# Kernel optimization log

Measured on AMD Instinct MI355X. Metric: run time of the kernel, lower is better.

The kernel has to match this reference:

```python
import jax, jax.numpy as jnp
import numpy as np

OUT = 7            # output_size per dim
RATIO = 2          # sampling_ratio
CANON_S = 160.0    # canonical_scale
CANON_L = 4.0      # canonical_level
EPS = 1e-6
K_MIN, K_MAX = 2, 5                      # from scales 1/4 .. 1/32
SCALES = (0.25, 0.125, 0.0625, 0.03125)  # inferred vs 256^3 image


def _coords(start, bsz):
    # start,bsz: [N] -> sample coords [N, OUT*RATIO]
    offs = (jnp.arange(OUT)[:, None] + (jnp.arange(RATIO) + 0.5) / RATIO).reshape(-1)
    return start[:, None] + offs[None, :] * bsz[:, None]


def _axis(c, dim):
    # torchvision border handling: zero outside [-1, dim], clamp inside
    valid = ((c > -1.0) & (c < dim)).astype(c.dtype)
    cc = jnp.clip(c, 0.0, dim - 1.0)
    lo = jnp.floor(cc).astype(jnp.int32)
    hi = jnp.minimum(lo + 1, int(dim) - 1)
    frac = cc - lo
    return lo, hi, (1.0 - frac) * valid, frac * valid


def roi_align_3d(feat, batch_idx, boxes, scale):
    # feat [B,C,X,Y,Z]; boxes [N,6] = (x1,y1,z1,x2,y2,z2) in image coords
    N = boxes.shape[0]
    C = feat.shape[1]
    dims = feat.shape[2:]
    start = boxes[:, :3] * scale
    size = jnp.maximum(boxes[:, 3:] * scale - start, 1.0)
    bsz = size / OUT  # [N,3] bin sizes
    f = jnp.transpose(feat, (0, 2, 3, 4, 1))  # [B,X,Y,Z,C]
    ax = [_axis(_coords(start[:, d], bsz[:, d]), float(dims[d])) for d in range(3)]
    b = batch_idx
    acc = jnp.zeros((N, OUT * RATIO, OUT * RATIO, OUT * RATIO, C), feat.dtype)
    for ix, wx in ((ax[0][0], ax[0][2]), (ax[0][1], ax[0][3])):
        for iy, wy in ((ax[1][0], ax[1][2]), (ax[1][1], ax[1][3])):
            for iz, wz in ((ax[2][0], ax[2][2]), (ax[2][1], ax[2][3])):
                v = f[b[:, None, None, None], ix[:, :, None, None],
                      iy[:, None, :, None], iz[:, None, None, :]]  # [N,Sx,Sy,Sz,C]
                w = wx[:, :, None, None] * wy[:, None, :, None] * wz[:, None, None, :]
                acc = acc + w[..., None] * v
    # average sampling points within each bin
    acc = acc.reshape(N, OUT, RATIO, OUT, RATIO, OUT, RATIO, C).mean(axis=(2, 4, 6))
    return jnp.transpose(acc, (0, 4, 1, 2, 3))  # [N,C,OUT,OUT,OUT]


def level_map(boxes):
    vol = ((boxes[:, 3] - boxes[:, 0]) * (boxes[:, 4] - boxes[:, 1])
           * (boxes[:, 5] - boxes[:, 2]))
    s = jnp.cbrt(vol)
    lvl = jnp.floor(CANON_L + jnp.log2(s / CANON_S) + EPS)
    return jnp.clip(lvl, K_MIN, K_MAX).astype(jnp.int32) - K_MIN


def setup_inputs() -> dict:
    key = jax.random.key(0)
    ks = jax.random.split(key, 6)
    N, C = 256, 64
    feat0 = jax.random.normal(ks[0], (1, C, 64, 64, 64), jnp.float32)
    feat1 = jax.random.normal(ks[1], (1, C, 32, 32, 32), jnp.float32)
    feat2 = jax.random.normal(ks[2], (1, C, 16, 16, 16), jnp.float32)
    feat3 = jax.random.normal(ks[3], (1, C, 8, 8, 8), jnp.float32)
    sz = 10.0 + jax.random.uniform(ks[4], (N, 3)) * 240.0   # edge lengths
    p1 = jax.random.uniform(ks[5], (N, 3)) * (256.0 - sz)
    boxes = jnp.concatenate([p1, p1 + sz], axis=1)  # valid (x1<x2 etc.) in 256^3 image
    return {"feat0": feat0, "feat1": feat1, "feat2": feat2, "feat3": feat3, "boxes": boxes}


def reference(feat0, feat1, feat2, feat3, boxes):
    feats = (feat0, feat1, feat2, feat3)
    levels = level_map(boxes)
    b = jnp.zeros(boxes.shape[0], dtype=jnp.int32)  # single image -> all batch id 0
    out = jnp.zeros((boxes.shape[0], feat0.shape[1], OUT, OUT, OUT), feat0.dtype)
    for l, (feat, sc) in enumerate(zip(feats, SCALES)):
        pooled = roi_align_3d(feat, b, boxes, sc)
        mask = (levels == l).astype(pooled.dtype)[:, None, None, None, None]
        out = out + mask * pooled
    return out
```

## Files before the change

### kernel.cpp

```cpp
#include <hip/hip_runtime.h>
#include <math.h>

#define OUT 7
#define NVOX 343
#define VB 32
#define NCH2 11

typedef unsigned short u16;
typedef unsigned int u32;

__device__ __forceinline__ u16 f32_to_bf16(float f) {
    u32 u = __float_as_uint(f);
    u32 r = (u + 0x7fffu + ((u >> 16) & 1u)) >> 16;
    return (u16)r;
}
__device__ __forceinline__ float bf16_to_f32(u16 h) {
    return __uint_as_float(((u32)h) << 16);
}

__device__ __forceinline__ void axis_samp(float c, float fdim, int dim,
                                          int& lo, float& w0, float& w1) {
    float valid = (c > -1.0f && c < fdim) ? 1.0f : 0.0f;
    float cc = fminf(fmaxf(c, 0.0f), fdim - 1.0f);
    lo = (int)floorf(cc);
    float fr = cc - (float)lo;
    w0 = (1.0f - fr) * valid;
    w1 = fr * valid;
}

__device__ __forceinline__ void box_setup(const float* bp,
                                          int d0, int d1, int d2_, int d3,
                                          int& l, int& dim, float& fdim,
                                          float& st0, float& st1, float& st2,
                                          float& bs0, float& bs1, float& bs2) {
    float b0 = bp[0], b1 = bp[1], b2 = bp[2];
    float b3 = bp[3], b4 = bp[4], b5 = bp[5];
    float vol = (b3 - b0) * (b4 - b1) * (b5 - b2);
    float s = cbrtf(vol);
    float lvl = floorf(4.0f + log2f(s / 160.0f) + 1e-6f);
    lvl = fminf(fmaxf(lvl, 2.0f), 5.0f);
    l = (int)lvl - 2;
    float scale;
    if (l == 0)      { dim = d0;  scale = 0.25f;    }
    else if (l == 1) { dim = d1;  scale = 0.125f;   }
    else if (l == 2) { dim = d2_; scale = 0.0625f;  }
    else             { dim = d3;  scale = 0.03125f; }
    fdim = (float)dim;
    st0 = b0 * scale; st1 = b1 * scale; st2 = b2 * scale;
    float e0 = fmaxf(b3 * scale - st0, 1.0f);
    float e1 = fmaxf(b4 * scale - st1, 1.0f);
    float e2 = fmaxf(b5 * scale - st2, 1.0f);
    bs0 = e0 * (1.0f / OUT); bs1 = e1 * (1.0f / OUT); bs2 = e2 * (1.0f / OUT);
}

#define LDSF 11776
#define FBLK 512

__global__ __launch_bounds__(FBLK) void roi_align_fallback_kernel(
    const float* __restrict__ f0, const float* __restrict__ f1,
    const float* __restrict__ f2, const float* __restrict__ f3,
    const float* __restrict__ boxes, float* __restrict__ out,
    int N, int C, int d0, int d1, int d2_, int d3)
{
    __shared__ float lds[LDSF];
    const int c   = blockIdx.x;
    const int n   = blockIdx.y;
    const int tid = threadIdx.x;

    int l, dim; float fdim, st0, st1, st2, bs0, bs1, bs2;
    box_setup(boxes + n * 6, d0, d1, d2_, d3,
              l, dim, fdim, st0, st1, st2, bs0, bs1, bs2);
    const float* f = (l == 0) ? f0 : (l == 1) ? f1 : (l == 2) ? f2 : f3;

    const int dsq = dim * dim;
    const size_t dcube = (size_t)dim * dsq;
    const float* fc = f + (size_t)c * dcube;

    int x0 = (int)floorf(fminf(fmaxf(st0 + 0.25f * bs0, 0.0f), fdim - 1.0f));
    int x1 = min((int)floorf(fminf(fmaxf(st0 + 6.75f * bs0, 0.0f), fdim - 1.0f)) + 1, dim - 1);
    int y0 = (int)floorf(fminf(fmaxf(st1 + 0.25f * bs1, 0.0f), fdim - 1.0f));
    int y1 = min((int)floorf(fminf(fmaxf(st1 + 6.75f * bs1, 0.0f), fdim - 1.0f)) + 1, dim - 1);
    int z0 = (int)floorf(fminf(fmaxf(st2 + 0.25f * bs2, 0.0f), fdim - 1.0f));
    int z1 = min((int)floorf(fminf(fmaxf(st2 + 6.75f * bs2, 0.0f), fdim - 1.0f)) + 1, dim - 1);

    int nx = x1 - x0 + 1, ny = y1 - y0 + 1, nz = z1 - z0 + 1;
    int nzp = nz + 1;
    int nynzp = ny * nzp;
    int nrows = nx * ny;
    int nregp = nrows * nzp;

    int xl[2], yl[2], zl[2];
    float xw0[2], xw1[2], yw0[2], yw1[2], zw0[2], zw1[2];
    if (tid < NVOX) {
        int oz = tid % OUT;
        int oy = (tid / OUT) % OUT;
        int ox = tid / (OUT * OUT);
        #pragma unroll
        for (int r = 0; r < 2; ++r) {
            float off = 0.25f + 0.5f * (float)r;
            axis_samp(st0 + ((float)ox + off) * bs0, fdim, dim, xl[r], xw0[r], xw1[r]);
            axis_samp(st1 + ((float)oy + off) * bs1, fdim, dim, yl[r], yw0[r], yw1[r]);
            axis_samp(st2 + ((float)oz + off) * bs2, fdim, dim, zl[r], zw0[r], zw1[r]);
        }
    }

    if (nregp <= LDSF) {
        float rnzp = 1.0f / (float)nzp;
        float rny  = 1.0f / (float)ny;
        for (int e = tid; e < nregp; e += FBLK) {
            int row = (int)((float)e * rnzp);
            int zz = e - row * nzp;
            if (zz < 0)        { row -= 1; zz += nzp; }
            else if (zz >= nzp){ row += 1; zz -= nzp; }
            int rx = (int)((float)row * rny);
            int ry = row - rx * ny;
            if (ry < 0)        { rx -= 1; ry += ny; }
            else if (ry >= ny) { rx += 1; ry -= ny; }
            int zsrc = min(zz, nz - 1);
            lds[e] = fc[((size_t)(x0 + rx) * dim + (y0 + ry)) * dim + (z0 + zsrc)];
        }
        __syncthreads();

        if (tid < NVOX) {
            int XL[2], XH[2], YL[2], YH[2], ZL[2];
            #pragma unroll
            for (int r = 0; r < 2; ++r) {
                XL[r] = (xl[r] - x0) * nynzp;
                XH[r] = (min(xl[r] + 1, dim - 1) - x0) * nynzp;
                YL[r] = (yl[r] - y0) * nzp;
                YH[r] = (min(yl[r] + 1, dim - 1) - y0) * nzp;
                ZL[r] = zl[r] - z0;
            }
            float acc = 0.0f;
            #pragma unroll
            for (int rx2 = 0; rx2 < 2; ++rx2) {
                #pragma unroll
                for (int ry2 = 0; ry2 < 2; ++ry2) {
                    #pragma unroll
                    for (int rz2 = 0; rz2 < 2; ++rz2) {
                        const float* pll = lds + (XL[rx2] + YL[ry2] + ZL[rz2]);
                        const float* plh = lds + (XL[rx2] + YH[ry2] + ZL[rz2]);
                        const float* phl = lds + (XH[rx2] + YL[ry2] + ZL[rz2]);
                        const float* phh = lds + (XH[rx2] + YH[ry2] + ZL[rz2]);
                        float wz0 = zw0[rz2], wz1 = zw1[rz2];
                        float vx0 = yw0[ry2] * (wz0 * pll[0] + wz1 * pll[1])
                                  + yw1[ry2] * (wz0 * plh[0] + wz1 * plh[1]);
                        float vx1 = yw0[ry2] * (wz0 * phl[0] + wz1 * phl[1])
                                  + yw1[ry2] * (wz0 * phh[0] + wz1 * phh[1]);
                        acc += xw0[rx2] * vx0 + xw1[rx2] * vx1;
                    }
                }
            }
            out[((size_t)n * C + c) * NVOX + tid] = acc * 0.125f;
        }
    } else {
        if (tid < NVOX) {
            float acc = 0.0f;
            #pragma unroll
            for (int rx2 = 0; rx2 < 2; ++rx2) {
                const float* pxl = fc + (size_t)xl[rx2] * dsq;
                const float* pxh = fc + (size_t)min(xl[rx2] + 1, dim - 1) * dsq;
                float wx0 = xw0[rx2], wx1 = xw1[rx2];
                #pragma unroll
                for (int ry2 = 0; ry2 < 2; ++ry2) {
                    int ryl = yl[ry2] * dim;
                    int ryh = min(yl[ry2] + 1, dim - 1) * dim;
                    float wy0 = yw0[ry2], wy1 = yw1[ry2];
                    #pragma unroll
                    for (int rz2 = 0; rz2 < 2; ++rz2) {
                        int bZL = zl[rz2], bZH = min(zl[rz2] + 1, dim - 1);
                        float wz0 = zw0[rz2], wz1 = zw1[rz2];
                        float vx0 = wy0 * (wz0 * pxl[ryl + bZL] + wz1 * pxl[ryl + bZH])
                                  + wy1 * (wz0 * pxl[ryh + bZL] + wz1 * pxl[ryh + bZH]);
                        float vx1 = wy0 * (wz0 * pxh[ryl + bZL] + wz1 * pxh[ryl + bZH])
                                  + wy1 * (wz0 * pxh[ryh + bZL] + wz1 * pxh[ryh + bZH]);
                        acc += wx0 * vx0 + wx1 * vx1;
                    }
                }
            }
            out[((size_t)n * C + c) * NVOX + tid] = acc * 0.125f;
        }
    }
}

__global__ __launch_bounds__(256) void transpose_bf16_kernel(
    const float* __restrict__ f0, const float* __restrict__ f1,
    const float* __restrict__ f2, const float* __restrict__ f3,
    u16* __restrict__ ws,
    int t1, int t2, int t3,
    long S0, long S1, long S2, long S3,
    long off0, long off1, long off2, long off3)
{
    __shared__ u16 tile[64 * 65];
    int b = blockIdx.x;
    const float* src; u16* dst; long S; int tloc;
    if (b < t1)      { src = f0; dst = ws + off0; S = S0; tloc = b; }
    else if (b < t2) { src = f1; dst = ws + off1; S = S1; tloc = b - t1; }
    else if (b < t3) { src = f2; dst = ws + off2; S = S2; tloc = b - t2; }
    else             { src = f3; dst = ws + off3; S = S3; tloc = b - t3; }

    long s0 = (long)tloc * 64;
    int lane  = threadIdx.x & 63;
    int chunk = threadIdx.x >> 6;
    #pragma unroll
    for (int k = 0; k < 16; ++k) {
        int ch = chunk * 16 + k;
        tile[lane * 65 + ch] = f32_to_bf16(src[(size_t)ch * S + s0 + lane]);
    }
    __syncthreads();
    #pragma unroll
    for (int k = 0; k < 16; ++k) {
        int s = chunk * 16 + k;
        dst[(s0 + s) * 64 + lane] = tile[s * 65 + lane];
    }
}


#define LSTRIDE 66

struct Grp { float w0, w1, w2, w3; ushort4 v0, v1, v2, v3; };

__device__ __forceinline__ Grp issue_grp(const int2* L, int g,
                                         const char* base, int qoff) {
    int4 a = *(const int4*)(L + (g << 2));
    int4 b = *(const int4*)(L + (g << 2) + 2);
    Grp r;
    r.w0 = __int_as_float(a.y); r.v0 = *(const ushort4*)(base + (a.x + qoff));
    r.w1 = __int_as_float(a.w); r.v1 = *(const ushort4*)(base + (a.z + qoff));
    r.w2 = __int_as_float(b.y); r.v2 = *(const ushort4*)(base + (b.x + qoff));
    r.w3 = __int_as_float(b.w); r.v3 = *(const ushort4*)(base + (b.z + qoff));
    return r;
}

__device__ __forceinline__ void consume_grp(const Grp& g, float4& acc) {
    acc.x = fmaf(g.w0, bf16_to_f32(g.v0.x), acc.x);
    acc.y = fmaf(g.w0, bf16_to_f32(g.v0.y), acc.y);
    acc.z = fmaf(g.w0, bf16_to_f32(g.v0.z), acc.z);
    acc.w = fmaf(g.w0, bf16_to_f32(g.v0.w), acc.w);
    acc.x = fmaf(g.w1, bf16_to_f32(g.v1.x), acc.x);
    acc.y = fmaf(g.w1, bf16_to_f32(g.v1.y), acc.y);
    acc.z = fmaf(g.w1, bf16_to_f32(g.v1.z), acc.z);
    acc.w = fmaf(g.w1, bf16_to_f32(g.v1.w), acc.w);
    acc.x = fmaf(g.w2, bf16_to_f32(g.v2.x), acc.x);
    acc.y = fmaf(g.w2, bf16_to_f32(g.v2.y), acc.y);
    acc.z = fmaf(g.w2, bf16_to_f32(g.v2.z), acc.z);
    acc.w = fmaf(g.w2, bf16_to_f32(g.v2.w), acc.w);
    acc.x = fmaf(g.w3, bf16_to_f32(g.v3.x), acc.x);
    acc.y = fmaf(g.w3, bf16_to_f32(g.v3.y), acc.y);
    acc.z = fmaf(g.w3, bf16_to_f32(g.v3.z), acc.z);
    acc.w = fmaf(g.w3, bf16_to_f32(g.v3.w), acc.w);
}

__global__ __launch_bounds__(512, 4) void roi_align_cl_kernel(
    const u16* __restrict__ ws, const float* __restrict__ boxes,
    float* __restrict__ out, int N, int C,
    int d0, int d1, int d2_, int d3,
    long off0, long off1, long off2, long off3)
{
    __shared__ __align__(16) int2 lst[VB * LSTRIDE];
    __shared__ int2  awo[VB][3][4];
    __shared__ int   axm[VB][3];
    __shared__ int   bxl[1];
    __shared__ float ldsout[64 * (VB + 1)];

    const int n    = blockIdx.x;
    const int cb   = blockIdx.y * VB;
    const int tid  = threadIdx.x;
    const int quad = tid & 15;
    const int slot = tid >> 4;

    if (tid < 96) {
        int l, dim; float fdim, st0, st1, st2, bs0, bs1, bs2;
        box_setup(boxes + n * 6, d0, d1, d2_, d3,
                  l, dim, fdim, st0, st1, st2, bs0, bs1, bs2);
        if (tid == 0) bxl[0] = l;
        const int dsq = dim * dim;

        const int s = tid & 31;
        const int a = tid >> 5;
        int v = min(cb + s, NVOX - 1);
        int o2 = v % OUT;
        int t7 = v / OUT;
        int o1 = t7 % OUT;
        int o0 = t7 / OUT;
        const int   strB = (a == 0) ? dsq * 128 : (a == 1) ? dim * 128 : 128;
        const float oA   = (a == 0) ? (float)o0 : (a == 1) ? (float)o1 : (float)o2;
        const float sA   = (a == 0) ? st0 : (a == 1) ? st1 : st2;
        const float bA   = (a == 0) ? bs0 : (a == 1) ? bs1 : bs2;
        const float sc   = (a == 0) ? 0.125f : 1.0f;

        int lo0, lo1; float w00, w01, w10, w11;
        axis_samp(sA + (oA + 0.25f) * bA, fdim, dim, lo0, w00, w01);
        axis_samp(sA + (oA + 0.75f) * bA, fdim, dim, lo1, w10, w11);
        int hi0 = min(lo0 + 1, dim - 1);
        int hi1 = min(lo1 + 1, dim - 1);
        int sa, sb; float qa, qb;
        if (hi0 <= lo1) { sa = hi0; qa = w01; sb = lo1; qb = w10; }
        else            { sa = lo1; qa = w10; sb = hi0; qb = w01; }
        int m = 0;
        int cur = lo0; float wacc = w00;
        if (sa == cur) wacc += qa;
        else {
            if (wacc > 0.0f) { awo[s][a][m] = make_int2(cur * strB, __float_as_int(wacc * sc)); ++m; }
            cur = sa; wacc = qa;
        }
        if (sb == cur) wacc += qb;
        else {
            if (wacc > 0.0f) { awo[s][a][m] = make_int2(cur * strB, __float_as_int(wacc * sc)); ++m; }
            cur = sb; wacc = qb;
        }
        if (hi1 == cur) wacc += w11;
        else {
            if (wacc > 0.0f) { awo[s][a][m] = make_int2(cur * strB, __float_as_int(wacc * sc)); ++m; }
            cur = hi1; wacc = w11;
        }
        if (wacc > 0.0f) { awo[s][a][m] = make_int2(cur * strB, __float_as_int(wacc * sc)); ++m; }
        axm[s][a] = m;
    }
    __syncthreads();

    const int l = bxl[0];
    const long loff = (l == 0) ? off0 : (l == 1) ? off1 : (l == 2) ? off2 : off3;
    int NTw;
    {
        const int mx = axm[slot][0], my = axm[slot][1], mz = axm[slot][2];
        const int myz = my * mz;
        const int nT  = mx * myz;
        int nT8 = (nT + 7) & ~7;
        int m1  = max(nT8, __shfl_xor(nT8, 16));
        NTw     = max(m1, __shfl_xor(m1, 32));
        const float rYZ = __builtin_amdgcn_rcpf((float)max(myz, 1));
        const float rZ  = __builtin_amdgcn_rcpf((float)max(mz, 1));
        for (int t = quad; t < NTw; t += 16) {
            int off = 0; float w = 0.0f;
            if (t < nT) {
                int i   = (int)(((float)t + 0.5f) * rYZ);
                int rem = t - i * myz;
                int j   = (int)(((float)rem + 0.5f) * rZ);
                int k   = rem - j * mz;
                int2 ei = awo[slot][0][i];
                int2 ej = awo[slot][1][j];
                int2 ek = awo[slot][2][k];
                w   = __int_as_float(ei.y) * __int_as_float(ej.y) * __int_as_float(ek.y);
                off = ei.x + ej.x + ek.x;
            }
            lst[slot * LSTRIDE + t] = make_int2(off, __float_as_int(w));
        }
    }

    {
        const char* base = (const char*)(ws + loff);
        const int qoff   = quad * 8;
        const int2* L    = lst + slot * LSTRIDE;
        const int NG     = NTw >> 2;
        float4 acc = { 0.f, 0.f, 0.f, 0.f };
        if (NG >= 2) {
            Grp A = issue_grp(L, 0, base, qoff);
            int g = 1;
            for (; g + 1 < NG; g += 2) {
                Grp B = issue_grp(L, g, base, qoff);
                consume_grp(A, acc);
                A = issue_grp(L, g + 1, base, qoff);
                consume_grp(B, acc);
            }
            Grp B = issue_grp(L, g, base, qoff);
            consume_grp(A, acc);
            consume_grp(B, acc);
        }
        int chb = quad * 4;
        ldsout[(chb + 0) * (VB + 1) + slot] = acc.x;
        ldsout[(chb + 1) * (VB + 1) + slot] = acc.y;
        ldsout[(chb + 2) * (VB + 1) + slot] = acc.z;
        ldsout[(chb + 3) * (VB + 1) + slot] = acc.w;
    }
    __syncthreads();

    const int nv = min(VB, NVOX - cb);
    #pragma unroll
    for (int k = 0; k < 4; ++k) {
        int flat = k * 512 + tid;
        int ch = flat >> 5, vs = flat & 31;
        if (vs < nv)
            out[((size_t)n * C + ch) * NVOX + cb + vs] = ldsout[ch * (VB + 1) + vs];
    }
}

extern "C" void kernel_launch(void* const* d_in, const int* in_sizes, int n_in,
                              void* d_out, int out_size, void* d_ws, size_t ws_size,
                              hipStream_t stream) {
    const float* f0 = (const float*)d_in[0];
    const float* f1 = (const float*)d_in[1];
    const float* f2 = (const float*)d_in[2];
    const float* f3 = (const float*)d_in[3];
    const float* boxes = (const float*)d_in[4];
    float* out = (float*)d_out;

    int N = in_sizes[4] / 6;
    int C = out_size / (N * NVOX);

    auto cdim = [&](int sz) {
        int per_c = sz / C;
        return (int)(cbrtf((float)per_c) + 0.5f);
    };
    int d0 = cdim(in_sizes[0]);
    int d1 = cdim(in_sizes[1]);
    int d2 = cdim(in_sizes[2]);
    int d3 = cdim(in_sizes[3]);

    long S0 = (long)d0 * d0 * d0, S1 = (long)d1 * d1 * d1;
    long S2 = (long)d2 * d2 * d2, S3 = (long)d3 * d3 * d3;
    long off0 = 0, off1 = S0 * C, off2 = off1 + S1 * C, off3 = off2 + S2 * C;
    size_t need = (size_t)(off3 + S3 * C) * sizeof(u16);

    bool fast = (C == 64) && (ws_size >= need) &&
                (S0 % 64 == 0) && (S1 % 64 == 0) && (S2 % 64 == 0) && (S3 % 64 == 0);

    if (fast) {
        u16* ws = (u16*)d_ws;
        int t1 = (int)(S0 / 64);
        int t2 = t1 + (int)(S1 / 64);
        int t3 = t2 + (int)(S2 / 64);
        int tt = t3 + (int)(S3 / 64);
        transpose_bf16_kernel<<<tt, 256, 0, stream>>>(f0, f1, f2, f3, ws,
                                                      t1, t2, t3,
                                                      S0, S1, S2, S3,
                                                      off0, off1, off2, off3);
        dim3 grid(N, NCH2);
        roi_align_cl_kernel<<<grid, 512, 0, stream>>>(ws, boxes, out, N, C,
                                                      d0, d1, d2, d3,
                                                      off0, off1, off2, off3);
    } else {
        dim3 grid(C, N);
        roi_align_fallback_kernel<<<grid, FBLK, 0, stream>>>(f0, f1, f2, f3, boxes, out,
                                                             N, C, d0, d1, d2, d3);
    }
}
```

Baseline: 146.8 us.

## Use 16-byte gathers with 8 channels per thread and drop LDS output staging

Each thread now gathers 8 bf16 channels per corner with a single 16-byte load instead of 4 channels with an 8-byte load. This halves the block to 256 threads, with 8 threads per voxel. The bf16 unpacking uses shift/mask directly on packed 32-bit words. The LDS transpose for the output and its barrier are removed, and each thread writes its 8 channels straight to global memory. The goal is fewer, wider gather instructions and less sync, at the cost of less parallelism per block and strided, uncoalesced output stores.

Result: faster. 143.2 us (-2.4%).

```diff
diff --git a/kernel.cpp b/kernel.cpp
--- a/kernel.cpp
+++ b/kernel.cpp
@@ -218,40 +218,36 @@
 
 #define LSTRIDE 66
 
-struct Grp { float w0, w1, w2, w3; ushort4 v0, v1, v2, v3; };
-
-__device__ __forceinline__ Grp issue_grp(const int2* L, int g,
-                                         const char* base, int qoff) {
+struct Grp8 { float w0, w1, w2, w3; uint4 v0, v1, v2, v3; };
+
+__device__ __forceinline__ Grp8 issue_grp8(const int2* L, int g,
+                                           const char* base, int qoff) {
     int4 a = *(const int4*)(L + (g << 2));
     int4 b = *(const int4*)(L + (g << 2) + 2);
-    Grp r;
-    r.w0 = __int_as_float(a.y); r.v0 = *(const ushort4*)(base + (a.x + qoff));
-    r.w1 = __int_as_float(a.w); r.v1 = *(const ushort4*)(base + (a.z + qoff));
-    r.w2 = __int_as_float(b.y); r.v2 = *(const ushort4*)(base + (b.x + qoff));
-    r.w3 = __int_as_float(b.w); r.v3 = *(const ushort4*)(base + (b.z + qoff));
+    Grp8 r;
+    r.w0 = __int_as_float(a.y); r.v0 = *(const uint4*)(base + (a.x + qoff));
+    r.w1 = __int_as_float(a.w); r.v1 = *(const uint4*)(base + (a.z + qoff));
+    r.w2 = __int_as_float(b.y); r.v2 = *(const uint4*)(base + (b.x + qoff));
+    r.w3 = __int_as_float(b.w); r.v3 = *(const uint4*)(base + (b.z + qoff));
     return r;
 }
 
-__device__ __forceinline__ void consume_grp(const Grp& g, float4& acc) {
-    acc.x = fmaf(g.w0, bf16_to_f32(g.v0.x), acc.x);
-    acc.y = fmaf(g.w0, bf16_to_f32(g.v0.y), acc.y);
-    acc.z = fmaf(g.w0, bf16_to_f32(g.v0.z), acc.z);
-    acc.w = fmaf(g.w0, bf16_to_f32(g.v0.w), acc.w);
-    acc.x = fmaf(g.w1, bf16_to_f32(g.v1.x), acc.x);
-    acc.y = fmaf(g.w1, bf16_to_f32(g.v1.y), acc.y);
-    acc.z = fmaf(g.w1, bf16_to_f32(g.v1.z), acc.z);
-    acc.w = fmaf(g.w1, bf16_to_f32(g.v1.w), acc.w);
-    acc.x = fmaf(g.w2, bf16_to_f32(g.v2.x), acc.x);
-    acc.y = fmaf(g.w2, bf16_to_f32(g.v2.y), acc.y);
-    acc.z = fmaf(g.w2, bf16_to_f32(g.v2.z), acc.z);
-    acc.w = fmaf(g.w2, bf16_to_f32(g.v2.w), acc.w);
-    acc.x = fmaf(g.w3, bf16_to_f32(g.v3.x), acc.x);
-    acc.y = fmaf(g.w3, bf16_to_f32(g.v3.y), acc.y);
-    acc.z = fmaf(g.w3, bf16_to_f32(g.v3.z), acc.z);
-    acc.w = fmaf(g.w3, bf16_to_f32(g.v3.w), acc.w);
-}
-
-__global__ __launch_bounds__(512, 4) void roi_align_cl_kernel(
+#define ACC2(u, w, aE, aO)                                          \
+    aE = fmaf(w, __uint_as_float((u) << 16), aE);                   \
+    aO = fmaf(w, __uint_as_float((u) & 0xffff0000u), aO);
+
+__device__ __forceinline__ void consume_grp8(const Grp8& g, float4& a0, float4& a1) {
+    ACC2(g.v0.x, g.w0, a0.x, a0.y)  ACC2(g.v0.y, g.w0, a0.z, a0.w)
+    ACC2(g.v0.z, g.w0, a1.x, a1.y)  ACC2(g.v0.w, g.w0, a1.z, a1.w)
+    ACC2(g.v1.x, g.w1, a0.x, a0.y)  ACC2(g.v1.y, g.w1, a0.z, a0.w)
+    ACC2(g.v1.z, g.w1, a1.x, a1.y)  ACC2(g.v1.w, g.w1, a1.z, a1.w)
+    ACC2(g.v2.x, g.w2, a0.x, a0.y)  ACC2(g.v2.y, g.w2, a0.z, a0.w)
+    ACC2(g.v2.z, g.w2, a1.x, a1.y)  ACC2(g.v2.w, g.w2, a1.z, a1.w)
+    ACC2(g.v3.x, g.w3, a0.x, a0.y)  ACC2(g.v3.y, g.w3, a0.z, a0.w)
+    ACC2(g.v3.z, g.w3, a1.x, a1.y)  ACC2(g.v3.w, g.w3, a1.z, a1.w)
+}
+
+__global__ __launch_bounds__(256, 4) void roi_align_cl_kernel(
     const u16* __restrict__ ws, const float* __restrict__ boxes,
     float* __restrict__ out, int N, int C,
     int d0, int d1, int d2_, int d3,
@@ -261,13 +257,12 @@
     __shared__ int2  awo[VB][3][4];
     __shared__ int   axm[VB][3];
     __shared__ int   bxl[1];
-    __shared__ float ldsout[64 * (VB + 1)];
 
     const int n    = blockIdx.x;
     const int cb   = blockIdx.y * VB;
     const int tid  = threadIdx.x;
-    const int quad = tid & 15;
-    const int slot = tid >> 4;
+    const int oct  = tid & 7;
+    const int slot = tid >> 3;
 
     if (tid < 96) {
         int l, dim; float fdim, st0, st1, st2, bs0, bs1, bs2;
@@ -327,11 +322,12 @@
         const int myz = my * mz;
         const int nT  = mx * myz;
         int nT8 = (nT + 7) & ~7;
-        int m1  = max(nT8, __shfl_xor(nT8, 16));
-        NTw     = max(m1, __shfl_xor(m1, 32));
+        int m1  = max(nT8, __shfl_xor(nT8, 8));
+        m1      = max(m1,  __shfl_xor(m1, 16));
+        NTw     = max(m1,  __shfl_xor(m1, 32));
         const float rYZ = __builtin_amdgcn_rcpf((float)max(myz, 1));
         const float rZ  = __builtin_amdgcn_rcpf((float)max(mz, 1));
-        for (int t = quad; t < NTw; t += 16) {
+        for (int t = oct; t < NTw; t += 8) {
             int off = 0; float w = 0.0f;
             if (t < nT) {
                 int i   = (int)(((float)t + 0.5f) * rYZ);
@@ -348,40 +344,35 @@
         }
     }
 
+    float4 a0 = { 0.f, 0.f, 0.f, 0.f };
+    float4 a1 = { 0.f, 0.f, 0.f, 0.f };
     {
         const char* base = (const char*)(ws + loff);
-        const int qoff   = quad * 8;
+        const int qoff   = oct * 16;
         const int2* L    = lst + slot * LSTRIDE;
         const int NG     = NTw >> 2;
-        float4 acc = { 0.f, 0.f, 0.f, 0.f };
         if (NG >= 2) {
-            Grp A = issue_grp(L, 0, base, qoff);
+            Grp8 A = issue_grp8(L, 0, base, qoff);
             int g = 1;
             for (; g + 1 < NG; g += 2) {
-                Grp B = issue_grp(L, g, base, qoff);
-                consume_grp(A, acc);
-                A = issue_grp(L, g + 1, base, qoff);
-                consume_grp(B, acc);
+                Grp8 B = issue_grp8(L, g, base, qoff);
+                consume_grp8(A, a0, a1);
+                A = issue_grp8(L, g + 1, base, qoff);
+                consume_grp8(B, a0, a1);
             }
-            Grp B = issue_grp(L, g, base, qoff);
-            consume_grp(A, acc);
-            consume_grp(B, acc);
-        }
-        int chb = quad * 4;
-        ldsout[(chb + 0) * (VB + 1) + slot] = acc.x;
-        ldsout[(chb + 1) * (VB + 1) + slot] = acc.y;
-        ldsout[(chb + 2) * (VB + 1) + slot] = acc.z;
-        ldsout[(chb + 3) * (VB + 1) + slot] = acc.w;
-    }
-    __syncthreads();
-
-    const int nv = min(VB, NVOX - cb);
-    #pragma unroll
-    for (int k = 0; k < 4; ++k) {
-        int flat = k * 512 + tid;
-        int ch = flat >> 5, vs = flat & 31;
-        if (vs < nv)
-            out[((size_t)n * C + ch) * NVOX + cb + vs] = ldsout[ch * (VB + 1) + vs];
+            Grp8 B = issue_grp8(L, g, base, qoff);
+            consume_grp8(A, a0, a1);
+            consume_grp8(B, a0, a1);
+        }
+    }
+
+    const int vox = cb + slot;
+    if (vox < NVOX) {
+        float* op = out + (size_t)n * C * NVOX + (size_t)(oct * 8) * NVOX + vox;
+        op[0 * NVOX] = a0.x;  op[1 * NVOX] = a0.y;
+        op[2 * NVOX] = a0.z;  op[3 * NVOX] = a0.w;
+        op[4 * NVOX] = a1.x;  op[5 * NVOX] = a1.y;
+        op[6 * NVOX] = a1.z;  op[7 * NVOX] = a1.w;
     }
 }
 
@@ -426,7 +417,7 @@
                                                       S0, S1, S2, S3,
                                                       off0, off1, off2, off3);
         dim3 grid(N, NCH2);
-        roi_align_cl_kernel<<<grid, 512, 0, stream>>>(ws, boxes, out, N, C,
+        roi_align_cl_kernel<<<grid, 256, 0, stream>>>(ws, boxes, out, N, C,
                                                       d0, d1, d2, d3,
                                                       off0, off1, off2, off3);
     } else {
```
